# Kernel tuning notes

Measured on AMD Instinct MI355X. Metric: run time of the kernel, lower is better.

The kernel has to match this reference:

```python
import jax, jax.numpy as jnp
import numpy as np

B, S, N = 1, 128, 256
C_IN, C_H, C_OUT = 256, 32, 128
EPS = 1e-5


def setup_inputs() -> dict:
    key = jax.random.key(0)
    k_m, k_wa, k_wb, k_wo = jax.random.split(key, 4)
    m = jax.random.normal(k_m, (B, S, N, C_IN), dtype=jnp.float32)
    mask = jnp.ones((B, S, N), dtype=jnp.float32)
    gamma = jnp.ones((C_IN,), dtype=jnp.float32)
    beta = jnp.zeros((C_IN,), dtype=jnp.float32)
    # nn.Linear weights are (out, in)
    Wa = jax.random.normal(k_wa, (C_H, C_IN), dtype=jnp.float32) / np.sqrt(C_IN).astype(np.float32)
    Wb = jax.random.normal(k_wb, (C_H, C_IN), dtype=jnp.float32) / np.sqrt(C_IN).astype(np.float32)
    # proj_o is final_init (zeros) in the source; use small random weights so the
    # baseline output is non-trivial for correctness checking.
    Wo = jax.random.normal(k_wo, (C_OUT, C_H * C_H), dtype=jnp.float32) / np.sqrt(C_H * C_H).astype(np.float32)
    bo = jnp.zeros((C_OUT,), dtype=jnp.float32)
    return {"m": m, "mask": mask, "gamma": gamma, "beta": beta,
            "Wa": Wa, "Wb": Wb, "Wo": Wo, "bo": bo}


def reference(m, mask, gamma, beta, Wa, Wb, Wo, bo):
    # LayerNorm over c_in
    mu = jnp.mean(m, axis=-1, keepdims=True)
    var = jnp.mean((m - mu) ** 2, axis=-1, keepdims=True)
    mn = (m - mu) * jax.lax.rsqrt(var + EPS) * gamma + beta  # (B,S,N,c_in)

    mk = mask[..., None]  # (B,S,N,1)
    a = jnp.einsum('bsni,hi->bsnh', mn, Wa) * mk  # (B,S,N,c_h)
    b = jnp.einsum('bsni,hi->bsnh', mn, Wb) * mk  # (B,S,N,c_h)

    # pairwise mask count over S, clamped to >= 1
    num_mask = jnp.clip(jnp.einsum('bsi,bsj->bij', mask, mask), 1.0, None)  # (B,N,N)

    # outer-product mean over the sequence dim
    z = jnp.einsum('bsic,bsjd->bijcd', a, b)  # (B,N,N,c_h,c_h)
    z = z.reshape(z.shape[0], z.shape[1], z.shape[2], C_H * C_H)
    z = z / num_mask[..., None]

    return jnp.einsum('bijk,ok->bijo', z, Wo) + bo  # (B,N,N,c_out)
```

## Files before the change

### kernel.cpp

```cpp
#include <hip/hip_runtime.h>
#include <hip/hip_bf16.h>

#define S_DIM 128
#define N_DIM 256
#define CIN   256
#define CH    32
#define COUT  128

typedef __attribute__((ext_vector_type(8))) short bf16x8;
typedef __attribute__((ext_vector_type(4))) float f32x4;
typedef __attribute__((ext_vector_type(16))) float f32x16;

__device__ __forceinline__ unsigned short f2bf(float f) {
  union { float f; unsigned int u; } v; v.f = f;
  unsigned int u = v.u;
  return (unsigned short)((u + 0x7FFFu + ((u >> 16) & 1u)) >> 16);
}

__device__ __forceinline__ unsigned int pk2(float x, float y) {
  float2 f2; f2.x = x; f2.y = y;
  __hip_bfloat162 h = __float22bfloat162_rn(f2);
  union { __hip_bfloat162 h; unsigned int u; } c; c.h = h;
  return c.u;
}

__global__ __launch_bounds__(256) void lnp_prep_kernel(
    const float* __restrict__ m, const float* __restrict__ mask,
    const float* __restrict__ gamma, const float* __restrict__ beta,
    const float* __restrict__ Wa, const float* __restrict__ Wb,
    const float* __restrict__ Wo,
    float* __restrict__ rnm, unsigned short* __restrict__ wo3,
    unsigned short* __restrict__ a_t, unsigned short* __restrict__ b_t) {
  const int b = blockIdx.x, t = threadIdx.x;
  if (b < 1024) {
    __shared__ __align__(16) unsigned short mn[32][264];
    __shared__ __align__(16) unsigned short wabs[64 * 256];
    const int i = b & 255, s0 = (b >> 8) * 32;
    const int w = t >> 6, l = t & 63, lq = l >> 4, lr = l & 15;

    #pragma unroll
    for (int it = 0; it < 8; it++) {
      const int gi = it * 256 + t;
      const int r = gi >> 5, g = gi & 31;
      const float* src = (r < 32) ? (Wa + r * 256 + g * 8)
                                  : (Wb + (r - 32) * 256 + g * 8);
      const int gp = (g & 16) | ((g ^ (r & 15)) & 15);
      const float4 v0 = *(const float4*)(src);
      const float4 v1 = *(const float4*)(src + 4);
      uint4 qv;
      qv.x = pk2(v0.x, v0.y); qv.y = pk2(v0.z, v0.w);
      qv.z = pk2(v1.x, v1.y); qv.w = pk2(v1.z, v1.w);
      *(uint4*)(&wabs[r * 256 + gp * 8]) = qv;
    }

    const float4 g4 = *(const float4*)(gamma + l * 4);
    const float4 b4 = *(const float4*)(beta + l * 4);

    float4 mv[8];
    float mkv[8];
    #pragma unroll
    for (int rr = 0; rr < 8; rr++) {
      const int s = s0 + w * 8 + rr;
      mv[rr] = *(const float4*)(m + ((size_t)(s * N_DIM + i)) * CIN + l * 4);
      mkv[rr] = mask[s * N_DIM + i];
    }

    #pragma unroll
    for (int rr = 0; rr < 8; rr++) {
      const int r = w * 8 + rr;
      const float4 v = mv[rr];
      float sum = v.x + v.y + v.z + v.w;
      float sq  = v.x * v.x + v.y * v.y + v.z * v.z + v.w * v.w;
      #pragma unroll
      for (int off = 32; off > 0; off >>= 1) {
        sum += __shfl_down(sum, off);
        sq  += __shfl_down(sq, off);
      }
      sum = __shfl(sum, 0); sq = __shfl(sq, 0);
      const float mu = sum * (1.0f / CIN);
      const float var = fmaxf(sq * (1.0f / CIN) - mu * mu, 0.0f);
      const float rs = rsqrtf(var + 1e-5f);
      const float mk = mkv[rr];
      uint2 p2;
      p2.x = pk2(((v.x - mu) * rs * g4.x + b4.x) * mk,
                 ((v.y - mu) * rs * g4.y + b4.y) * mk);
      p2.y = pk2(((v.z - mu) * rs * g4.z + b4.z) * mk,
                 ((v.w - mu) * rs * g4.w + b4.w) * mk);
      *(uint2*)(&mn[r][l * 4]) = p2;
    }
    __syncthreads();

    const int wm = w & 1;
    const int n2 = w >> 1;
    f32x4 acc0 = {0.f, 0.f, 0.f, 0.f}, acc1 = {0.f, 0.f, 0.f, 0.f};
    #pragma unroll
    for (int ks = 0; ks < 8; ks++) {
      const int k0 = ks * 32 + lq * 8;
      const int g = ks * 4 + lq;
      const int gp = (g & 16) | ((g ^ lr) & 15);
      const bf16x8 af = *(const bf16x8*)(&mn[wm * 16 + lr][k0]);
      const bf16x8 bf0 = *(const bf16x8*)(&wabs[(n2 * 32 + lr) * 256 + gp * 8]);
      const bf16x8 bf1 = *(const bf16x8*)(&wabs[(n2 * 32 + 16 + lr) * 256 + gp * 8]);
      acc0 = __builtin_amdgcn_mfma_f32_16x16x32_bf16(af, bf0, acc0, 0, 0, 0);
      acc1 = __builtin_amdgcn_mfma_f32_16x16x32_bf16(af, bf1, acc1, 0, 0, 0);
    }

    unsigned short* dst = (n2 == 0) ? a_t : b_t;
    const int scol = s0 + wm * 16 + lq * 4;
    uint2 q0, q1;
    q0.x = pk2(acc0[0], acc0[1]); q0.y = pk2(acc0[2], acc0[3]);
    q1.x = pk2(acc1[0], acc1[1]); q1.y = pk2(acc1[2], acc1[3]);
    *(uint2*)(dst + ((size_t)(i * CH + lr)) * S_DIM + scol) = q0;
    *(uint2*)(dst + ((size_t)(i * CH + 16 + lr)) * S_DIM + scol) = q1;
  } else if (b < 1152) {
    const int r = b - 1024;
    #pragma unroll
    for (int q = 0; q < 4; q++) {
      const int f = r * 1024 + q * 256 + t;
      const int e = f & 7, l = (f >> 3) & 63;
      const int step = (f >> 9) & 63, og = f >> 15;
      const int kp = step * 16 + (l >> 5) * 8 + e;
      const int c = kp & 31, d = kp >> 5;
      const int o = og * 32 + (l & 31);
      wo3[f] = f2bf(Wo[o * 1024 + c * 32 + d]);
    }
  } else {
    const int i = b - 1152;
    float acc = 0.f;
    #pragma unroll 8
    for (int s = 0; s < S_DIM; s++)
      acc += mask[s * N_DIM + i] * mask[s * N_DIM + t];
    acc = fmaxf(acc, 1.0f);
    rnm[i * N_DIM + t] = 1.0f / acc;
  }
}

__global__ __launch_bounds__(512, 4) void fused_kernel(
    const unsigned short* __restrict__ a_t, const unsigned short* __restrict__ b_t,
    const unsigned short* __restrict__ wo3, const float* __restrict__ rnm,
    const float* __restrict__ bo, float* __restrict__ out) {
  extern __shared__ __align__(16) unsigned short smem[];
  unsigned short* sA0 = smem;
  unsigned short* sA1 = smem + 8192;
  unsigned short* sB0 = smem + 16384;
  unsigned short* sB1 = smem + 20480;
  unsigned short* sZ = smem;
  float* fpart = (float*)smem;

  const int t = threadIdx.x, w = t >> 6, l = t & 63;
  const int lq = l >> 4, lr = l & 15;
  const int bx = blockIdx.x, by = blockIdx.y;

  const unsigned short* srcA = a_t + (size_t)bx * 32768;
  const unsigned short* srcB = b_t + (size_t)by * 16384;

  const int og = w & 3, kh = w >> 2;
  const int pA = l & 31;
  const unsigned short* wop =
      wo3 + ((size_t)(og * 64 + kh * 32) * 64 + l) * 8;

  const int wy = (w >> 1) * 64, wx = (w & 1) * 64;
  f32x4 acc[4][4];
  #pragma unroll
  for (int a = 0; a < 4; a++)
    #pragma unroll
    for (int c = 0; c < 4; c++) acc[a][c] = (f32x4){0.f, 0.f, 0.f, 0.f};

  bf16x8 ldA0, ldA1, ldB0;
  const int sr = t >> 2, sg = t & 3;
  const int swz = ((sg ^ sr) & 3) << 3;

#define ISSUE_CH(c) do { \
    ldA0 = *(const bf16x8*)(srcA + sr * 128 + (c) * 32 + sg * 8); \
    ldA1 = *(const bf16x8*)(srcA + (128 + sr) * 128 + (c) * 32 + sg * 8); \
    ldB0 = *(const bf16x8*)(srcB + sr * 128 + (c) * 32 + sg * 8); \
  } while (0)

#define WRITE_CH(c) do { \
    unsigned short* dA = ((c) & 1) ? sA1 : sA0; \
    unsigned short* dB = ((c) & 1) ? sB1 : sB0; \
    *(bf16x8*)(&dA[sr * 32 + swz]) = ldA0; \
    *(bf16x8*)(&dA[(128 + sr) * 32 + swz]) = ldA1; \
    *(bf16x8*)(&dB[sr * 32 + swz]) = ldB0; \
  } while (0)

#define COMPUTE_CH(c) do { \
    const unsigned short* pa = ((c) & 1) ? sA1 : sA0; \
    const unsigned short* pb = ((c) & 1) ? sB1 : sB0; \
    bf16x8 afr[4], bfr[4]; \
    _Pragma("unroll") \
    for (int a2 = 0; a2 < 4; a2++) { \
      const int ra = wy + a2 * 16 + lr; \
      afr[a2] = *(const bf16x8*)(&pa[ra * 32 + (((lq ^ ra) & 3) << 3)]); \
      const int rb = wx + a2 * 16 + lr; \
      bfr[a2] = *(const bf16x8*)(&pb[rb * 32 + (((lq ^ rb) & 3) << 3)]); \
    } \
    _Pragma("unroll") \
    for (int a2 = 0; a2 < 4; a2++) \
      _Pragma("unroll") \
      for (int c2 = 0; c2 < 4; c2++) \
        acc[a2][c2] = __builtin_amdgcn_mfma_f32_16x16x32_bf16(afr[a2], bfr[c2], acc[a2][c2], 0, 0, 0); \
  } while (0)

  ISSUE_CH(0);
  WRITE_CH(0);
  ISSUE_CH(1);
  __syncthreads();

  WRITE_CH(1); ISSUE_CH(2); COMPUTE_CH(0); __syncthreads();
  WRITE_CH(2); ISSUE_CH(3); COMPUTE_CH(1); __syncthreads();
  WRITE_CH(3);              COMPUTE_CH(2); __syncthreads();

  bf16x8 wfb0[4], wfb1[4];
  #pragma unroll
  for (int q = 0; q < 4; q++)
    wfb0[q] = *(const bf16x8*)(wop + (size_t)q * 512);

  COMPUTE_CH(3);
  __syncthreads();

#undef ISSUE_CH
#undef WRITE_CH
#undef COMPUTE_CH

  #pragma unroll
  for (int a = 0; a < 4; a++) {
    #pragma unroll
    for (int c = 0; c < 4; c++) {
      const int zrb = wy + a * 16 + lq * 4;
      const int zc  = wx + c * 16 + lr;
      const int pr = (zrb >> 5) * 4 + (zc >> 5);
      const int off = (zc & 31) * 32 + (zrb & 31);
      const int g = off >> 3;
      const int gp = (g & ~7) | ((g ^ (g >> 3) ^ pr) & 7);
      uint2 q;
      q.x = pk2(acc[a][c][0], acc[a][c][1]);
      q.y = pk2(acc[a][c][2], acc[a][c][3]);
      *(uint2*)(&sZ[pr * 1024 + gp * 8 + (off & 7)]) = q;
    }
  }
  __syncthreads();

  #pragma unroll
  for (int q = 0; q < 4; q++)
    wfb1[q] = *(const bf16x8*)(wop + (size_t)(4 + q) * 512);

  const int pair = t >> 4;
  const int ob   = (t & 15) * 8;
  const int ii = bx * 8 + (pair >> 2), jj = by * 4 + (pair & 3);
  const float sc = rnm[ii * N_DIM + jj];
  const float4 bo0 = *(const float4*)(bo + ob);
  const float4 bo1 = *(const float4*)(bo + ob + 4);

  f32x16 acc2;
  #pragma unroll
  for (int r = 0; r < 16; r++) acc2[r] = 0.f;

  #pragma unroll
  for (int jb = 0; jb < 8; jb++) {
    #pragma unroll
    for (int q = 0; q < 4; q++) {
      const int j = jb * 4 + q;
      const int s = kh * 32 + j;
      const int g = s * 2 + (l >> 5);
      const int gA = (g & ~7) | ((g ^ (g >> 3) ^ pA) & 7);
      const bf16x8 zf = *(const bf16x8*)(&sZ[pA * 1024 + gA * 8]);
      const bf16x8 wf = (jb & 1) ? wfb1[q] : wfb0[q];
      acc2 = __builtin_amdgcn_mfma_f32_32x32x16_bf16(zf, wf, acc2, 0, 0, 0);
    }
    if (jb < 6) {
      #pragma unroll
      for (int q = 0; q < 4; q++) {
        const bf16x8 v = *(const bf16x8*)(wop + (size_t)((jb + 2) * 4 + q) * 512);
        if (jb & 1) wfb1[q] = v; else wfb0[q] = v;
      }
    }
  }
  __syncthreads();

  const int oc = og * 32 + (l & 31);
  #pragma unroll
  for (int r = 0; r < 16; r++) {
    const int row = (r & 3) + 8 * (r >> 2) + 4 * (l >> 5);
    fpart[kh * 4224 + row * 132 + oc] = acc2[r];
  }
  __syncthreads();

  const int fb = pair * 132 + ob;
  f32x4 u0 = {0.f, 0.f, 0.f, 0.f}, u1 = {0.f, 0.f, 0.f, 0.f};
  #pragma unroll
  for (int q = 0; q < 2; q++) {
    u0 += *(const f32x4*)(&fpart[q * 4224 + fb]);
    u1 += *(const f32x4*)(&fpart[q * 4224 + fb + 4]);
  }
  float* po = out + ((size_t)(ii * N_DIM + jj)) * COUT + ob;
  float4 w0, w1;
  w0.x = u0[0] * sc + bo0.x; w0.y = u0[1] * sc + bo0.y;
  w0.z = u0[2] * sc + bo0.z; w0.w = u0[3] * sc + bo0.w;
  w1.x = u1[0] * sc + bo1.x; w1.y = u1[1] * sc + bo1.y;
  w1.z = u1[2] * sc + bo1.z; w1.w = u1[3] * sc + bo1.w;
  *(float4*)(po)     = w0;
  *(float4*)(po + 4) = w1;
}

extern "C" void kernel_launch(void* const* d_in, const int* in_sizes, int n_in,
                              void* d_out, int out_size, void* d_ws, size_t ws_size,
                              hipStream_t stream) {
  const float* m     = (const float*)d_in[0];
  const float* mask  = (const float*)d_in[1];
  const float* gamma = (const float*)d_in[2];
  const float* beta  = (const float*)d_in[3];
  const float* Wa    = (const float*)d_in[4];
  const float* Wb    = (const float*)d_in[5];
  const float* Wo    = (const float*)d_in[6];
  const float* bo    = (const float*)d_in[7];
  float* out = (float*)d_out;

  char* ws = (char*)d_ws;
  float*          rnm = (float*)(ws);
  unsigned short* wo3 = (unsigned short*)(ws + 262144);
  unsigned short* a_t = (unsigned short*)(ws + 524288);
  unsigned short* b_t = (unsigned short*)(ws + 2621440);

  hipFuncSetAttribute((const void*)fused_kernel,
                      hipFuncAttributeMaxDynamicSharedMemorySize, 65536);

  lnp_prep_kernel<<<1408, 256, 0, stream>>>(m, mask, gamma, beta, Wa, Wb, Wo,
                                            rnm, wo3, a_t, b_t);
  fused_kernel<<<dim3(32, 64), 512, 65536, stream>>>(a_t, b_t, wo3, rnm, bo, out);
}
```

Before: 154.8 us.

## Stream operand tiles directly into LDS with a triple-buffered async pipeline

Replaces register-staged global loads plus LDS stores with global_load_lds direct-to-LDS transfers. The LDS ring grows from two buffers to three, and synchronisation uses explicit vmcnt waits and raw barriers. The swizzle pattern changes so that the direct writes stay conflict-free. This is meant to remove the register round trip and VGPR pressure and to overlap more loading with MFMA work. The cost is more dynamic shared memory (72KB vs 64KB), which may reduce the number of resident blocks per CU.

```diff
diff --git a/kernel.cpp b/kernel.cpp
--- a/kernel.cpp
+++ b/kernel.cpp
@@ -22,6 +22,12 @@
   __hip_bfloat162 h = __float22bfloat162_rn(f2);
   union { __hip_bfloat162 h; unsigned int u; } c; c.h = h;
   return c.u;
+}
+
+__device__ __forceinline__ void gld16(const unsigned short* g, unsigned short* l) {
+  __builtin_amdgcn_global_load_lds(
+      (const __attribute__((address_space(1))) unsigned int*)g,
+      (__attribute__((address_space(3))) unsigned int*)l, 16, 0, 0);
 }
 
 __global__ __launch_bounds__(256) void lnp_prep_kernel(
@@ -142,8 +148,10 @@
   extern __shared__ __align__(16) unsigned short smem[];
   unsigned short* sA0 = smem;
   unsigned short* sA1 = smem + 8192;
-  unsigned short* sB0 = smem + 16384;
-  unsigned short* sB1 = smem + 20480;
+  unsigned short* sA2 = smem + 16384;
+  unsigned short* sB0 = smem + 24576;
+  unsigned short* sB1 = smem + 28672;
+  unsigned short* sB2 = smem + 32768;
   unsigned short* sZ = smem;
   float* fpart = (float*)smem;
 
@@ -166,61 +174,66 @@
     #pragma unroll
     for (int c = 0; c < 4; c++) acc[a][c] = (f32x4){0.f, 0.f, 0.f, 0.f};
 
-  bf16x8 ldA0, ldA1, ldB0;
-  const int sr = t >> 2, sg = t & 3;
-  const int swz = ((sg ^ sr) & 3) << 3;
-
-#define ISSUE_CH(c) do { \
-    ldA0 = *(const bf16x8*)(srcA + sr * 128 + (c) * 32 + sg * 8); \
-    ldA1 = *(const bf16x8*)(srcA + (128 + sr) * 128 + (c) * 32 + sg * 8); \
-    ldB0 = *(const bf16x8*)(srcB + sr * 128 + (c) * 32 + sg * 8); \
+  const int ra0 = t >> 2,         ga0 = t & 3;
+  const int ra1 = (512 + t) >> 2, ga1 = t & 3;
+  const int rb0 = t >> 2,         gb0 = t & 3;
+
+#define ISSUE_CH(c, bufA, bufB) do {                                          \
+    gld16(srcA + ra0 * 128 + (c) * 32 + ((ga0 ^ ((ra0 >> 2) & 3)) << 3),      \
+          bufA + t * 8);                                                      \
+    gld16(srcA + ra1 * 128 + (c) * 32 + ((ga1 ^ ((ra1 >> 2) & 3)) << 3),      \
+          bufA + (512 + t) * 8);                                              \
+    gld16(srcB + rb0 * 128 + (c) * 32 + ((gb0 ^ ((rb0 >> 2) & 3)) << 3),      \
+          bufB + t * 8);                                                      \
   } while (0)
 
-#define WRITE_CH(c) do { \
-    unsigned short* dA = ((c) & 1) ? sA1 : sA0; \
-    unsigned short* dB = ((c) & 1) ? sB1 : sB0; \
-    *(bf16x8*)(&dA[sr * 32 + swz]) = ldA0; \
-    *(bf16x8*)(&dA[(128 + sr) * 32 + swz]) = ldA1; \
-    *(bf16x8*)(&dB[sr * 32 + swz]) = ldB0; \
-  } while (0)
-
-#define COMPUTE_CH(c) do { \
-    const unsigned short* pa = ((c) & 1) ? sA1 : sA0; \
-    const unsigned short* pb = ((c) & 1) ? sB1 : sB0; \
-    bf16x8 afr[4], bfr[4]; \
-    _Pragma("unroll") \
-    for (int a2 = 0; a2 < 4; a2++) { \
-      const int ra = wy + a2 * 16 + lr; \
-      afr[a2] = *(const bf16x8*)(&pa[ra * 32 + (((lq ^ ra) & 3) << 3)]); \
-      const int rb = wx + a2 * 16 + lr; \
-      bfr[a2] = *(const bf16x8*)(&pb[rb * 32 + (((lq ^ rb) & 3) << 3)]); \
-    } \
-    _Pragma("unroll") \
-    for (int a2 = 0; a2 < 4; a2++) \
-      _Pragma("unroll") \
-      for (int c2 = 0; c2 < 4; c2++) \
+#define COMPUTE_CH(bufA, bufB) do {                                           \
+    bf16x8 afr[4], bfr[4];                                                    \
+    _Pragma("unroll")                                                         \
+    for (int a2 = 0; a2 < 4; a2++) {                                          \
+      const int ra = wy + a2 * 16 + lr;                                       \
+      afr[a2] = *(const bf16x8*)(&(bufA)[ra * 32 + ((lq ^ ((ra >> 2) & 3)) << 3)]); \
+      const int rb = wx + a2 * 16 + lr;                                       \
+      bfr[a2] = *(const bf16x8*)(&(bufB)[rb * 32 + ((lq ^ ((rb >> 2) & 3)) << 3)]); \
+    }                                                                         \
+    _Pragma("unroll")                                                         \
+    for (int a2 = 0; a2 < 4; a2++)                                            \
+      _Pragma("unroll")                                                       \
+      for (int c2 = 0; c2 < 4; c2++)                                          \
         acc[a2][c2] = __builtin_amdgcn_mfma_f32_16x16x32_bf16(afr[a2], bfr[c2], acc[a2][c2], 0, 0, 0); \
   } while (0)
 
-  ISSUE_CH(0);
-  WRITE_CH(0);
-  ISSUE_CH(1);
-  __syncthreads();
-
-  WRITE_CH(1); ISSUE_CH(2); COMPUTE_CH(0); __syncthreads();
-  WRITE_CH(2); ISSUE_CH(3); COMPUTE_CH(1); __syncthreads();
-  WRITE_CH(3);              COMPUTE_CH(2); __syncthreads();
+  ISSUE_CH(0, sA0, sB0);
+  ISSUE_CH(1, sA1, sB1);
+  asm volatile("s_waitcnt vmcnt(0)" ::: "memory");
+  __builtin_amdgcn_s_barrier();
+  __builtin_amdgcn_sched_barrier(0);
+
+  ISSUE_CH(2, sA2, sB2);
+  COMPUTE_CH(sA0, sB0);
+  asm volatile("s_waitcnt vmcnt(3)" ::: "memory");
+  __builtin_amdgcn_s_barrier();
+  __builtin_amdgcn_sched_barrier(0);
+
+  ISSUE_CH(3, sA0, sB0);
+  COMPUTE_CH(sA1, sB1);
+  asm volatile("s_waitcnt vmcnt(3)" ::: "memory");
+  __builtin_amdgcn_s_barrier();
+  __builtin_amdgcn_sched_barrier(0);
 
   bf16x8 wfb0[4], wfb1[4];
   #pragma unroll
   for (int q = 0; q < 4; q++)
     wfb0[q] = *(const bf16x8*)(wop + (size_t)q * 512);
-
-  COMPUTE_CH(3);
+  COMPUTE_CH(sA2, sB2);
+  asm volatile("s_waitcnt vmcnt(4)" ::: "memory");
+  __builtin_amdgcn_s_barrier();
+  __builtin_amdgcn_sched_barrier(0);
+
+  COMPUTE_CH(sA0, sB0);
   __syncthreads();
 
 #undef ISSUE_CH
-#undef WRITE_CH
 #undef COMPUTE_CH
 
   #pragma unroll
@@ -323,9 +336,9 @@
   unsigned short* b_t = (unsigned short*)(ws + 2621440);
 
   hipFuncSetAttribute((const void*)fused_kernel,
-                      hipFuncAttributeMaxDynamicSharedMemorySize, 65536);
+                      hipFuncAttributeMaxDynamicSharedMemorySize, 73728);
 
   lnp_prep_kernel<<<1408, 256, 0, stream>>>(m, mask, gamma, beta, Wa, Wb, Wo,
                                             rnm, wo3, a_t, b_t);
-  fused_kernel<<<dim3(32, 64), 512, 65536, stream>>>(a_t, b_t, wo3, rnm, bo, out);
-}
+  fused_kernel<<<dim3(32, 64), 512, 73728, stream>>>(a_t, b_t, wo3, rnm, bo, out);
+}
```

New measurement: 151.1 us. 2.4% less time.
